# Kernel tuning notes

Measured on AMD Instinct MI355X. Metric: run time of the kernel, lower is better.

The kernel has to match this reference:

```python
import jax, jax.numpy as jnp
import numpy as np
from jax import lax

EPS = 1e-06
B, T, F = 32, 8192, 128


def setup_inputs() -> dict:
    key = jax.random.key(0)
    k1, k2 = jax.random.split(key)
    x = jax.random.uniform(k1, (B, T, F), dtype=jnp.float32)
    state = jax.random.uniform(k2, (B, 1, F), dtype=jnp.float32)
    log_s = jnp.log(jnp.full((F,), 0.025, dtype=jnp.float32))
    log_alpha = jnp.log(jnp.full((F,), 0.98, dtype=jnp.float32))
    log_delta = jnp.log(jnp.full((F,), 2.0, dtype=jnp.float32))
    log_r = jnp.log(jnp.full((F,), 0.5, dtype=jnp.float32))
    return {"x": x, "state": state, "log_s": log_s, "log_alpha": log_alpha,
            "log_delta": log_delta, "log_r": log_r}


def reference(x, state, log_s, log_alpha, log_delta, log_r):
    # per-channel gains, broadcast over (B, T, F)
    s = jnp.exp(log_s)          # (F,)
    alpha = jnp.exp(log_alpha)  # (F,)
    delta = jnp.exp(log_delta)  # (F,)
    r = jnp.exp(log_r)          # (F,)

    carry0 = state[:, 0, :]  # (B, F)

    def step(c, xt):
        c = (1.0 - s) * c + s * xt  # (B, F)
        return c, c

    # scan over time: xs are (T, B, F)
    final_state, E = lax.scan(step, carry0, jnp.swapaxes(x, 0, 1))
    E = jnp.swapaxes(E, 0, 1)  # (B, T, F)

    y = (x / (EPS + E) ** alpha + delta) ** r - delta ** r
    new_state = final_state[:, None, :]  # (B, 1, F)
    return y, new_state
```

## Files before the change

kernel.cpp:

```cpp
#include <hip/hip_runtime.h>
#include <math.h>

#define EPS 1e-6f

constexpr int B_ = 32;
constexpr int T_ = 8192;
constexpr int F_ = 128;
constexpr int FG = F_ / 4;

__device__ __forceinline__ float fastpow(float b, float e) {
    return exp2f(e * __log2f(b));
}

template<int NC>
__global__ __launch_bounds__(256) void pcen_pass1(
    const float4* __restrict__ x4,
    const float*  __restrict__ log_s,
    float4* __restrict__ S4)
{
    constexpr int L = T_ / NC;
    const int fg    = threadIdx.x & 31;
    const int slot  = threadIdx.x >> 5;
    const int cb    = blockIdx.x % (NC / 8);
    const int b     = blockIdx.x / (NC / 8);
    const int chunk = cb * 8 + slot;

    const float4 lsv = reinterpret_cast<const float4*>(log_s)[fg];
    const float s0 = expf(lsv.x), s1 = expf(lsv.y), s2 = expf(lsv.z), s3 = expf(lsv.w);
    const float a0 = 1.f - s0,   a1 = 1.f - s1,    a2 = 1.f - s2,    a3 = 1.f - s3;

    const float4* xp = x4 + ((size_t)b * T_ + (size_t)chunk * L) * FG + fg;

    float c0 = 0.f, c1 = 0.f, c2 = 0.f, c3 = 0.f;
    #pragma unroll 8
    for (int i = 0; i < L; ++i) {
        const float4 xv = xp[(size_t)i * FG];
        c0 = fmaf(a0, c0, s0 * xv.x);
        c1 = fmaf(a1, c1, s1 * xv.y);
        c2 = fmaf(a2, c2, s2 * xv.z);
        c3 = fmaf(a3, c3, s3 * xv.w);
    }
    S4[((size_t)b * NC + chunk) * FG + fg] = make_float4(c0, c1, c2, c3);
}

template<int NC>
__global__ __launch_bounds__(32) void pcen_pass2(
    const float4* __restrict__ state4,
    const float*  __restrict__ log_s,
    const float4* __restrict__ S4,
    float4* __restrict__ carry4,
    float4* __restrict__ new_state4)
{
    constexpr int L = T_ / NC;
    const int fg = threadIdx.x;
    const int b  = blockIdx.x;

    const float4 lsv = reinterpret_cast<const float4*>(log_s)[fg];
    const float aL0 = powf(1.f - expf(lsv.x), (float)L);
    const float aL1 = powf(1.f - expf(lsv.y), (float)L);
    const float aL2 = powf(1.f - expf(lsv.z), (float)L);
    const float aL3 = powf(1.f - expf(lsv.w), (float)L);

    float4 c = state4[(size_t)b * FG + fg];
    for (int k = 0; k < NC; ++k) {
        const size_t idx = ((size_t)b * NC + k) * FG + fg;
        carry4[idx] = c;
        const float4 Sv = S4[idx];
        c.x = fmaf(aL0, c.x, Sv.x);
        c.y = fmaf(aL1, c.y, Sv.y);
        c.z = fmaf(aL2, c.z, Sv.z);
        c.w = fmaf(aL3, c.w, Sv.w);
    }
    new_state4[(size_t)b * FG + fg] = c;
}

template<int NC>
__global__ __launch_bounds__(256) void pcen_pass3(
    const float4* __restrict__ x4,
    const float*  __restrict__ log_s,
    const float*  __restrict__ log_alpha,
    const float*  __restrict__ log_delta,
    const float*  __restrict__ log_r,
    const float4* __restrict__ carry4,
    float4* __restrict__ y4)
{
    constexpr int L = T_ / NC;
    const int fg    = threadIdx.x & 31;
    const int slot  = threadIdx.x >> 5;
    const int cb    = blockIdx.x % (NC / 8);
    const int b     = blockIdx.x / (NC / 8);
    const int chunk = cb * 8 + slot;

    const float4 lsv = reinterpret_cast<const float4*>(log_s)[fg];
    const float4 lav = reinterpret_cast<const float4*>(log_alpha)[fg];
    const float4 ldv = reinterpret_cast<const float4*>(log_delta)[fg];
    const float4 lrv = reinterpret_cast<const float4*>(log_r)[fg];

    const float s0 = expf(lsv.x), s1 = expf(lsv.y), s2 = expf(lsv.z), s3 = expf(lsv.w);
    const float a0 = 1.f - s0,   a1 = 1.f - s1,    a2 = 1.f - s2,    a3 = 1.f - s3;
    const float na0 = -expf(lav.x), na1 = -expf(lav.y), na2 = -expf(lav.z), na3 = -expf(lav.w);
    const float d0 = expf(ldv.x), d1 = expf(ldv.y), d2 = expf(ldv.z), d3 = expf(ldv.w);
    const float r0 = expf(lrv.x), r1 = expf(lrv.y), r2 = expf(lrv.z), r3 = expf(lrv.w);
    const float dr0 = fastpow(d0, r0), dr1 = fastpow(d1, r1);
    const float dr2 = fastpow(d2, r2), dr3 = fastpow(d3, r3);

    float4 c = carry4[((size_t)b * NC + chunk) * FG + fg];

    const size_t base = ((size_t)b * T_ + (size_t)chunk * L) * FG + fg;
    const float4* xp = x4 + base;
    float4*       yp = y4 + base;

    #pragma unroll 4
    for (int i = 0; i < L; ++i) {
        const float4 xv = xp[(size_t)i * FG];

        c.x = fmaf(a0, c.x, s0 * xv.x);
        c.y = fmaf(a1, c.y, s1 * xv.y);
        c.z = fmaf(a2, c.z, s2 * xv.z);
        c.w = fmaf(a3, c.w, s3 * xv.w);

        const float u0 = xv.x * exp2f(na0 * __log2f(EPS + c.x));
        const float u1 = xv.y * exp2f(na1 * __log2f(EPS + c.y));
        const float u2 = xv.z * exp2f(na2 * __log2f(EPS + c.z));
        const float u3 = xv.w * exp2f(na3 * __log2f(EPS + c.w));

        float4 yv;
        yv.x = exp2f(r0 * __log2f(u0 + d0)) - dr0;
        yv.y = exp2f(r1 * __log2f(u1 + d1)) - dr1;
        yv.z = exp2f(r2 * __log2f(u2 + d2)) - dr2;
        yv.w = exp2f(r3 * __log2f(u3 + d3)) - dr3;

        yp[(size_t)i * FG] = yv;
    }
}

template<int NC>
static void launch_all(const float* x, const float* state,
                       const float* log_s, const float* log_alpha,
                       const float* log_delta, const float* log_r,
                       float* y, float* new_state, float* ws, hipStream_t stream)
{
    const float4* x4      = (const float4*)x;
    const float4* state4  = (const float4*)state;
    float4* y4            = (float4*)y;
    float4* new_state4    = (float4*)new_state;
    float4* S4            = (float4*)ws;
    float4* carry4        = S4 + (size_t)B_ * NC * FG;

    dim3 blk(256);
    dim3 grid13(B_ * (NC / 8));

    pcen_pass1<NC><<<grid13, blk, 0, stream>>>(x4, log_s, S4);
    pcen_pass2<NC><<<dim3(B_), dim3(32), 0, stream>>>(state4, log_s, S4, carry4, new_state4);
    pcen_pass3<NC><<<grid13, blk, 0, stream>>>(x4, log_s, log_alpha, log_delta, log_r, carry4, y4);
}

extern "C" void kernel_launch(void* const* d_in, const int* in_sizes, int n_in,
                              void* d_out, int out_size, void* d_ws, size_t ws_size,
                              hipStream_t stream)
{
    const float* x         = (const float*)d_in[0];
    const float* state     = (const float*)d_in[1];
    const float* log_s     = (const float*)d_in[2];
    const float* log_alpha = (const float*)d_in[3];
    const float* log_delta = (const float*)d_in[4];
    const float* log_r     = (const float*)d_in[5];

    float* y         = (float*)d_out;
    float* new_state = y + (size_t)B_ * T_ * F_;

    const size_t need128 = 2ull * B_ * 128 * F_ * sizeof(float);
    if (ws_size >= need128) {
        launch_all<128>(x, state, log_s, log_alpha, log_delta, log_r,
                        y, new_state, (float*)d_ws, stream);
    } else {
        launch_all<64>(x, state, log_s, log_alpha, log_delta, log_r,
                       y, new_state, (float*)d_ws, stream);
    }
}
```

Before: 87.38 us.

## Fuse carry scan into output pass and use nontemporal stores for y

Removes the serial single-warp pass2 kernel. Each thread in the output pass now recomputes its chunk's starting carry by scanning the preceding chunk summaries, using a precomputed (1-s)^L. This drops one kernel launch, the carry workspace and the serial 32-block bottleneck, in exchange for redundant prefix work (up to NC iterations per thread). It also raises the unroll factor of pass1, writes y with nontemporal stores to avoid cache pollution, and halves the workspace requirement.

```diff
diff --git a/kernel.cpp b/kernel.cpp
--- a/kernel.cpp
+++ b/kernel.cpp
@@ -8,7 +8,9 @@
 constexpr int F_ = 128;
 constexpr int FG = F_ / 4;
 
-__device__ __forceinline__ float fastpow(float b, float e) {
+typedef float f32x4 __attribute__((ext_vector_type(4)));
+
+__device__ __forceinline__ float fpow(float b, float e) {
     return exp2f(e * __log2f(b));
 }
 
@@ -32,7 +34,7 @@
     const float4* xp = x4 + ((size_t)b * T_ + (size_t)chunk * L) * FG + fg;
 
     float c0 = 0.f, c1 = 0.f, c2 = 0.f, c3 = 0.f;
-    #pragma unroll 8
+    #pragma unroll 16
     for (int i = 0; i < L; ++i) {
         const float4 xv = xp[(size_t)i * FG];
         c0 = fmaf(a0, c0, s0 * xv.x);
@@ -44,45 +46,16 @@
 }
 
 template<int NC>
-__global__ __launch_bounds__(32) void pcen_pass2(
+__global__ __launch_bounds__(256) void pcen_fused(
+    const float4* __restrict__ x4,
     const float4* __restrict__ state4,
-    const float*  __restrict__ log_s,
-    const float4* __restrict__ S4,
-    float4* __restrict__ carry4,
-    float4* __restrict__ new_state4)
-{
-    constexpr int L = T_ / NC;
-    const int fg = threadIdx.x;
-    const int b  = blockIdx.x;
-
-    const float4 lsv = reinterpret_cast<const float4*>(log_s)[fg];
-    const float aL0 = powf(1.f - expf(lsv.x), (float)L);
-    const float aL1 = powf(1.f - expf(lsv.y), (float)L);
-    const float aL2 = powf(1.f - expf(lsv.z), (float)L);
-    const float aL3 = powf(1.f - expf(lsv.w), (float)L);
-
-    float4 c = state4[(size_t)b * FG + fg];
-    for (int k = 0; k < NC; ++k) {
-        const size_t idx = ((size_t)b * NC + k) * FG + fg;
-        carry4[idx] = c;
-        const float4 Sv = S4[idx];
-        c.x = fmaf(aL0, c.x, Sv.x);
-        c.y = fmaf(aL1, c.y, Sv.y);
-        c.z = fmaf(aL2, c.z, Sv.z);
-        c.w = fmaf(aL3, c.w, Sv.w);
-    }
-    new_state4[(size_t)b * FG + fg] = c;
-}
-
-template<int NC>
-__global__ __launch_bounds__(256) void pcen_pass3(
-    const float4* __restrict__ x4,
     const float*  __restrict__ log_s,
     const float*  __restrict__ log_alpha,
     const float*  __restrict__ log_delta,
     const float*  __restrict__ log_r,
-    const float4* __restrict__ carry4,
-    float4* __restrict__ y4)
+    const float4* __restrict__ S4,
+    float4* __restrict__ y4,
+    float4* __restrict__ new_state4)
 {
     constexpr int L = T_ / NC;
     const int fg    = threadIdx.x & 31;
@@ -92,23 +65,35 @@
     const int chunk = cb * 8 + slot;
 
     const float4 lsv = reinterpret_cast<const float4*>(log_s)[fg];
+    const float s0 = expf(lsv.x), s1 = expf(lsv.y), s2 = expf(lsv.z), s3 = expf(lsv.w);
+    const float a0 = 1.f - s0,   a1 = 1.f - s1,    a2 = 1.f - s2,    a3 = 1.f - s3;
+
+    const float aL0 = fpow(a0, (float)L);
+    const float aL1 = fpow(a1, (float)L);
+    const float aL2 = fpow(a2, (float)L);
+    const float aL3 = fpow(a3, (float)L);
+
+    float4 c = state4[(size_t)b * FG + fg];
+    for (int k = 0; k < chunk; ++k) {
+        const float4 Sv = S4[((size_t)b * NC + k) * FG + fg];
+        c.x = fmaf(aL0, c.x, Sv.x);
+        c.y = fmaf(aL1, c.y, Sv.y);
+        c.z = fmaf(aL2, c.z, Sv.z);
+        c.w = fmaf(aL3, c.w, Sv.w);
+    }
+
     const float4 lav = reinterpret_cast<const float4*>(log_alpha)[fg];
     const float4 ldv = reinterpret_cast<const float4*>(log_delta)[fg];
     const float4 lrv = reinterpret_cast<const float4*>(log_r)[fg];
-
-    const float s0 = expf(lsv.x), s1 = expf(lsv.y), s2 = expf(lsv.z), s3 = expf(lsv.w);
-    const float a0 = 1.f - s0,   a1 = 1.f - s1,    a2 = 1.f - s2,    a3 = 1.f - s3;
     const float na0 = -expf(lav.x), na1 = -expf(lav.y), na2 = -expf(lav.z), na3 = -expf(lav.w);
     const float d0 = expf(ldv.x), d1 = expf(ldv.y), d2 = expf(ldv.z), d3 = expf(ldv.w);
     const float r0 = expf(lrv.x), r1 = expf(lrv.y), r2 = expf(lrv.z), r3 = expf(lrv.w);
-    const float dr0 = fastpow(d0, r0), dr1 = fastpow(d1, r1);
-    const float dr2 = fastpow(d2, r2), dr3 = fastpow(d3, r3);
-
-    float4 c = carry4[((size_t)b * NC + chunk) * FG + fg];
+    const float dr0 = fpow(d0, r0), dr1 = fpow(d1, r1);
+    const float dr2 = fpow(d2, r2), dr3 = fpow(d3, r3);
 
     const size_t base = ((size_t)b * T_ + (size_t)chunk * L) * FG + fg;
     const float4* xp = x4 + base;
-    float4*       yp = y4 + base;
+    f32x4*        yp = reinterpret_cast<f32x4*>(y4) + base;
 
     #pragma unroll 4
     for (int i = 0; i < L; ++i) {
@@ -124,13 +109,19 @@
         const float u2 = xv.z * exp2f(na2 * __log2f(EPS + c.z));
         const float u3 = xv.w * exp2f(na3 * __log2f(EPS + c.w));
 
-        float4 yv;
+        f32x4 yv;
         yv.x = exp2f(r0 * __log2f(u0 + d0)) - dr0;
         yv.y = exp2f(r1 * __log2f(u1 + d1)) - dr1;
         yv.z = exp2f(r2 * __log2f(u2 + d2)) - dr2;
         yv.w = exp2f(r3 * __log2f(u3 + d3)) - dr3;
 
-        yp[(size_t)i * FG] = yv;
+        __builtin_nontemporal_store(yv, &yp[(size_t)i * FG]);
+    }
+
+    if (chunk == NC - 1) {
+        float4 cs;
+        cs.x = c.x; cs.y = c.y; cs.z = c.z; cs.w = c.w;
+        new_state4[(size_t)b * FG + fg] = cs;
     }
 }
 
@@ -145,14 +136,13 @@
     float4* y4            = (float4*)y;
     float4* new_state4    = (float4*)new_state;
     float4* S4            = (float4*)ws;
-    float4* carry4        = S4 + (size_t)B_ * NC * FG;
 
     dim3 blk(256);
-    dim3 grid13(B_ * (NC / 8));
+    dim3 grid(B_ * (NC / 8));
 
-    pcen_pass1<NC><<<grid13, blk, 0, stream>>>(x4, log_s, S4);
-    pcen_pass2<NC><<<dim3(B_), dim3(32), 0, stream>>>(state4, log_s, S4, carry4, new_state4);
-    pcen_pass3<NC><<<grid13, blk, 0, stream>>>(x4, log_s, log_alpha, log_delta, log_r, carry4, y4);
+    pcen_pass1<NC><<<grid, blk, 0, stream>>>(x4, log_s, S4);
+    pcen_fused<NC><<<grid, blk, 0, stream>>>(x4, state4, log_s, log_alpha,
+                                             log_delta, log_r, S4, y4, new_state4);
 }
 
 extern "C" void kernel_launch(void* const* d_in, const int* in_sizes, int n_in,
@@ -169,7 +159,7 @@
     float* y         = (float*)d_out;
     float* new_state = y + (size_t)B_ * T_ * F_;
 
-    const size_t need128 = 2ull * B_ * 128 * F_ * sizeof(float);
+    const size_t need128 = (size_t)B_ * 128 * F_ * sizeof(float);
     if (ws_size >= need128) {
         launch_all<128>(x, state, log_s, log_alpha, log_delta, log_r,
                         y, new_state, (float*)d_ws, stream);
```

Result: slower. 99.72 us (+14.1%).
